# Kernel optimization log

Measured on AMD Instinct MI355X. Metric: run time of the kernel, lower is better.

## Reference

```python
import jax, jax.numpy as jnp
import numpy as np

B, P, G = 16, 16000, 256          # images, RPN proposals, gt boxes per image
S = 512                           # batch_size_per_image
POS_FRAC = 0.25
FG_T, BG_T = 0.5, 0.5             # fg/bg IoU thresholds
NUM_CLASSES = 91
BOX_W = jnp.array([10.0, 10.0, 5.0, 5.0], jnp.float32)  # box_coder weights
BETA = 1.0 / 9.0                  # smooth_l1 beta


def _make_boxes(k, n, img=800.0, maxwh=200.0):
    k1, k2 = jax.random.split(k)
    xy = jax.random.uniform(k1, (B, n, 2)) * img
    wh = jax.random.uniform(k2, (B, n, 2)) * maxwh + 1.0
    return jnp.concatenate([xy, xy + wh], -1)


def setup_inputs() -> dict:
    key = jax.random.key(0)
    ks = jax.random.split(key, 6)
    proposals = _make_boxes(ks[0], P)
    gt_boxes = _make_boxes(ks[1], G)
    gt_labels = jax.random.randint(ks[2], (B, G), 1, NUM_CLASSES)
    gt_thetas = jax.random.uniform(ks[3], (B, G)) * np.pi
    class_logits = jax.random.normal(ks[4], (B * S, NUM_CLASSES))
    box_regression = jax.random.normal(ks[5], (B * S, NUM_CLASSES * 5))
    return dict(class_logits=class_logits, box_regression=box_regression,
                proposals=proposals, gt_boxes=gt_boxes,
                gt_thetas=gt_thetas, gt_labels=gt_labels)


def _box_iou(a, b):
    # a: [G,4] gt, b: [M,4] proposals -> [G,M]
    area_a = (a[:, 2] - a[:, 0]) * (a[:, 3] - a[:, 1])
    area_b = (b[:, 2] - b[:, 0]) * (b[:, 3] - b[:, 1])
    lt = jnp.maximum(a[:, None, :2], b[None, :, :2])
    rb = jnp.minimum(a[:, None, 2:], b[None, :, 2:])
    wh = jnp.clip(rb - lt, 0.0)
    inter = wh[..., 0] * wh[..., 1]
    return inter / (area_a[:, None] + area_b[None, :] - inter)


def _encode(ref, prop):
    pw = prop[:, 2] - prop[:, 0]; ph = prop[:, 3] - prop[:, 1]
    px = prop[:, 0] + 0.5 * pw;   py = prop[:, 1] + 0.5 * ph
    gw = ref[:, 2] - ref[:, 0];   gh = ref[:, 3] - ref[:, 1]
    gx = ref[:, 0] + 0.5 * gw;    gy = ref[:, 1] + 0.5 * gh
    t = jnp.stack([(gx - px) / pw, (gy - py) / ph,
                   jnp.log(gw / pw), jnp.log(gh / ph)], 1)
    return t * BOX_W[None, :]


def _select_training_samples(props, gtb, gtl, gtt):
    # add_gt_proposals
    props_all = jnp.concatenate([props, gtb], 0)        # [P+G,4]
    # assign_targets_to_proposals (Matcher, allow_low_quality=False)
    iou = _box_iou(gtb, props_all)                      # [G,P+G]
    vals = iou.max(0)
    matches = iou.argmax(0)                             # clamped matched idxs
    below = vals < BG_T
    between = (vals >= BG_T) & (vals < FG_T)
    lbl = gtl[matches]
    lbl = jnp.where(below, 0, lbl)      # background
    lbl = jnp.where(between, -1, lbl)   # ignored
    # BalancedPositiveNegativeSampler (deterministic first-k variant)
    pos = lbl > 0
    neg = lbl == 0
    n_pos = jnp.minimum(pos.sum(), int(S * POS_FRAC))
    sel_pos = pos & (jnp.cumsum(pos) <= n_pos)
    sel_neg = neg & (jnp.cumsum(neg) <= (S - n_pos))
    mask = sel_pos | sel_neg
    sampled = jnp.argsort((~mask).astype(jnp.int32), stable=True)[:S]  # sorted selected idxs
    props_s = props_all[sampled]
    lbl_s = lbl[sampled]
    m = matches[sampled]
    reg = _encode(gtb[m], props_s)                       # [S,4]
    reg_t = jnp.concatenate([reg, gtt[m][:, None]], 1)   # append theta -> [S,5]
    return lbl_s, reg_t


def _fastrcnn_loss(class_logits, box_regression, labels, reg_targets):
    N = class_logits.shape[0]
    logp = jax.nn.log_softmax(class_logits, -1)
    cls_loss = -jnp.take_along_axis(logp, labels[:, None], 1).mean()
    br = box_regression.reshape(N, -1, 5)
    idx = jnp.broadcast_to(labels[:, None, None], (N, 1, 5))
    pred = jnp.take_along_axis(br, idx, axis=1)[:, 0, :]
    d = pred - reg_targets
    ad = jnp.abs(d)
    sl1 = jnp.where(ad < BETA, 0.5 * d * d / BETA, ad - 0.5 * BETA)
    pos = (labels > 0).astype(sl1.dtype)
    box_loss = jnp.sum(sl1 * pos[:, None]) / N
    return jnp.stack([cls_loss, box_loss])


def reference(class_logits, box_regression, proposals, gt_boxes, gt_thetas, gt_labels):
    labels, reg_t = jax.vmap(_select_training_samples)(proposals, gt_boxes, gt_labels, gt_thetas)
    labels = labels.reshape(-1)
    reg_t = reg_t.reshape(-1, 5)
    return _fastrcnn_loss(class_logits, box_regression, labels, reg_t)
```

## Files before the change

### kernel.cpp

```cpp
#include <hip/hip_runtime.h>

#define NB 16
#define NP 16000
#define NG 256
#define NM (NP + NG)
#define NSTRIP 254
#define NS 512
#define NCLS 91
#define SL1_BETA (1.0f/9.0f)
#define LOSS_BLOCKS 512

__global__ __launch_bounds__(256) void match_kernel(
    const float4* __restrict__ props4,
    const float4* __restrict__ gt4,
    const int*    __restrict__ gt_labels,
    unsigned int* __restrict__ posinfo)
{
    __shared__ float4   gbox[NG];
    __shared__ float    gar[NG];
    __shared__ int      glab[NG];
    __shared__ unsigned qst[256][5];

    const int b   = blockIdx.y;
    const int tid = threadIdx.x;

    {
        const float4 v = gt4[(size_t)b * NG + tid];
        gbox[tid] = v;
        gar[tid]  = (v.z - v.x) * (v.w - v.y);
        glab[tid] = gt_labels[b * NG + tid];
    }
    __syncthreads();

    const int h     = tid & 1;
    const int p     = tid >> 1;
    const int j     = blockIdx.x * 128 + p;
    const int gbase = h * 128;

    const float4 pb = (j < NP) ? props4[(size_t)b * NP + j]
                               : gt4[(size_t)b * NG + (j - NP)];
    const float ap = (pb.z - pb.x) * (pb.w - pb.y);

    int qcnt = 0, gf = -1;
    for (int w = 0; w < 4; ++w) {
        unsigned m = 0;
        #pragma unroll
        for (int t = 0; t < 32; ++t) {
            const int g = gbase + w * 32 + t;
            const float4 gb = gbox[g];
            const float  ga = gar[g];
            float lx = fmaxf(gb.x, pb.x), ly = fmaxf(gb.y, pb.y);
            float rx = fminf(gb.z, pb.z), ry = fminf(gb.w, pb.w);
            float ww = fmaxf(rx - lx, 0.0f), hh = fmaxf(ry - ly, 0.0f);
            float inter = ww * hh;
            float tt = ga + ap;
            if (fmaf(inter, 3.0f, -tt) >= 0.0f) m |= (1u << t);
        }
        qst[tid][w] = m;
        if (qcnt == 0 && m) gf = w * 32 + (__ffs(m) - 1);
        qcnt += __popc(m);
    }

    float ib = -1.0f, ub = 1.0f;
    int   gstar = -1;
    if (qcnt == 1) {
        const int g = gbase + gf;
        const float4 gb = gbox[g];
        float lx = fmaxf(gb.x, pb.x), ly = fmaxf(gb.y, pb.y);
        float rx = fminf(gb.z, pb.z), ry = fminf(gb.w, pb.w);
        float ww = fmaxf(rx - lx, 0.0f), hh = fmaxf(ry - ly, 0.0f);
        ib = ww * hh;
        ub = (gar[g] + ap) - ib;
        gstar = g;
    } else if (qcnt > 1) {
        for (int w = 0; w < 4; ++w) {
            unsigned m = qst[tid][w];
            while (m) {
                int t = __ffs(m) - 1; m &= m - 1;
                int g = gbase + w * 32 + t;
                const float4 gb = gbox[g];
                float lx = fmaxf(gb.x, pb.x), ly = fmaxf(gb.y, pb.y);
                float rx = fminf(gb.z, pb.z), ry = fminf(gb.w, pb.w);
                float ww = fmaxf(rx - lx, 0.0f), hh = fmaxf(ry - ly, 0.0f);
                float inter = ww * hh;
                float u = (gar[g] + ap) - inter;
                if (inter * ub > ib * u) { ib = inter; ub = u; gstar = g; }
            }
        }
    }

    const int   oq  = __shfl_xor(qcnt, 1, 64);
    const float oib = __shfl_xor(ib, 1, 64);
    const float oub = __shfl_xor(ub, 1, 64);
    const int   og  = __shfl_xor(gstar, 1, 64);
    const int qtot = qcnt + oq;
    int gm;
    if (qcnt > 0 && oq > 0) {
        bool otherWins;
        if (h == 0) otherWins = (oib * ub > ib * oub);
        else        otherWins = !(ib * oub > oib * ub);
        gm = otherWins ? og : gstar;
    } else {
        gm = (qcnt > 0) ? gstar : og;
    }

    if (h == 0) {
        unsigned info = 0;
        if (qtot > 0) info = ((unsigned)gm << 16) | (unsigned)glab[gm];
        posinfo[(size_t)b * NM + j] = info;
    }
}

__global__ __launch_bounds__(256) void sample_kernel(
    const float4* __restrict__ props4,
    const float4* __restrict__ gt4,
    const float*  __restrict__ gt_thetas,
    const unsigned int* __restrict__ posinfo,
    int*   __restrict__ labels_out,
    float* __restrict__ regt_out)
{
    __shared__ int sampled[NS];
    __shared__ int wsum[4];

    const int b    = blockIdx.x;
    const int tid  = threadIdx.x;
    const int lane = tid & 63;
    const int wid  = tid >> 6;
    const unsigned* P = posinfo + (size_t)b * NM;
    const int base = tid * 64;

    unsigned long long pm = 0ull;
    int cn = 0;
    if (tid < NSTRIP) {
        const uint4* Pv = reinterpret_cast<const uint4*>(P + base);
        #pragma unroll
        for (int q = 0; q < 16; ++q) {
            uint4 v = Pv[q];
            int e = q * 4;
            if (v.x) pm |= 1ull << (e + 0);
            if (v.y) pm |= 1ull << (e + 1);
            if (v.z) pm |= 1ull << (e + 2);
            if (v.w) pm |= 1ull << (e + 3);
        }
        cn = 64 - __popcll(pm);
    }
    int cp = (tid < NSTRIP) ? __popcll(pm) : 0;
    int val  = (cp << 16) | cn;
    int incl = val;
    #pragma unroll
    for (int off = 1; off < 64; off <<= 1) {
        int u = __shfl_up(incl, off, 64);
        if (lane >= off) incl += u;
    }
    if (lane == 63) wsum[wid] = incl;
    __syncthreads();
    int wbase = 0;
    #pragma unroll
    for (int w = 0; w < 4; ++w) if (w < wid) wbase += wsum[w];
    int tot  = wsum[0] + wsum[1] + wsum[2] + wsum[3];
    int excl = wbase + incl - val;
    int rp = excl >> 16, rn = excl & 0xffff;
    int posT = tot >> 16, negT = tot & 0xffff;
    int np = posT < 128 ? posT : 128;
    int nn = NS - np; if (nn > negT) nn = negT;

    if (tid < NSTRIP) {
        #pragma unroll 4
        for (int e = 0; e < 64; ++e) {
            int idx = base + e;
            if ((pm >> e) & 1ull) {
                if (rp < np) sampled[rp + (rn < nn ? rn : nn)] = idx;
                rp++;
            } else {
                if (rn < nn) sampled[rn + (rp < np ? rp : np)] = idx;
                rn++;
            }
        }
    }
    __syncthreads();
    if (tid == 0 && np + nn < NS) {
        int cpp = 0, cnn = 0, i = np + nn;
        for (int idx = 0; idx < NM && i < NS; ++idx) {
            bool p = P[idx] != 0;
            bool sel;
            if (p) { sel = cpp < np; cpp++; } else { sel = cnn < nn; cnn++; }
            if (!sel) sampled[i++] = idx;
        }
    }
    __syncthreads();

    for (int i = tid; i < NS; i += 256) {
        int idx = sampled[i];
        unsigned info = P[idx];
        int lbl = 0;
        if (info) {
            int m = info >> 16; lbl = info & 0xffff;
            float4 pv = (idx < NP) ? props4[(size_t)b * NP + idx]
                                   : gt4[(size_t)b * NG + (idx - NP)];
            float4 rv = gt4[(size_t)b * NG + m];
            float pw = pv.z - pv.x, ph = pv.w - pv.y;
            float px = pv.x + 0.5f * pw, py = pv.y + 0.5f * ph;
            float gw = rv.z - rv.x, gh = rv.w - rv.y;
            float gx = rv.x + 0.5f * gw, gy = rv.y + 0.5f * gh;
            float* o = regt_out + ((size_t)b * NS + i) * 5;
            o[0] = 10.0f * (gx - px) / pw;
            o[1] = 10.0f * (gy - py) / ph;
            o[2] = 5.0f * logf(gw / pw);
            o[3] = 5.0f * logf(gh / ph);
            o[4] = gt_thetas[b * NG + m];
        }
        labels_out[b * NS + i] = lbl;
    }
}

__global__ __launch_bounds__(256) void loss_kernel(
    const float* __restrict__ logits,
    const float* __restrict__ boxreg,
    const int*   __restrict__ labels,
    const float* __restrict__ regt,
    float2* __restrict__ partials)
{
    const int wave  = threadIdx.x >> 6;
    const int lane  = threadIdx.x & 63;
    const int gwave = blockIdx.x * 4 + wave;
    const int NWAVE = LOSS_BLOCKS * 4;
    const int N     = NB * NS;

    float cls_acc = 0.0f, box_acc = 0.0f;

    for (int r = gwave; r < N; r += NWAVE) {
        const float* row = logits + (size_t)r * NCLS;
        float a = (lane < NCLS)      ? row[lane]      : -3.0e38f;
        float c = (lane + 64 < NCLS) ? row[lane + 64] : -3.0e38f;
        float mx = fmaxf(a, c);
        #pragma unroll
        for (int o = 32; o; o >>= 1) mx = fmaxf(mx, __shfl_xor(mx, o, 64));
        float ssum = 0.0f;
        if (lane < NCLS)      ssum += expf(a - mx);
        if (lane + 64 < NCLS) ssum += expf(c - mx);
        #pragma unroll
        for (int o = 32; o; o >>= 1) ssum += __shfl_xor(ssum, o, 64);

        int lab = labels[r];
        float xl = (lab < 64) ? __shfl(a, lab, 64) : __shfl(c, lab - 64, 64);
        if (lane == 0) cls_acc += -(xl - mx - logf(ssum));

        if (lab > 0) {
            float d = 0.0f;
            if (lane < 5) {
                float pv = boxreg[(size_t)r * (NCLS * 5) + lab * 5 + lane];
                float tv = regt[(size_t)r * 5 + lane];
                d = pv - tv;
            }
            float ad = fabsf(d);
            float sl = (ad < SL1_BETA) ? 0.5f * d * d / SL1_BETA : ad - 0.5f * SL1_BETA;
            sl += __shfl_xor(sl, 4, 8);
            sl += __shfl_xor(sl, 2, 8);
            sl += __shfl_xor(sl, 1, 8);
            if (lane == 0) box_acc += sl;
        }
    }

    __shared__ float cpart[4], bpart[4];
    if (lane == 0) { cpart[wave] = cls_acc; bpart[wave] = box_acc; }
    __syncthreads();
    if (threadIdx.x == 0) {
        partials[blockIdx.x] = make_float2(cpart[0] + cpart[1] + cpart[2] + cpart[3],
                                           bpart[0] + bpart[1] + bpart[2] + bpart[3]);
    }
}

__global__ void final_kernel(const float2* __restrict__ partials,
                             float* __restrict__ out)
{
    const int tid  = threadIdx.x;
    const int lane = tid & 63;
    const int wid  = tid >> 6;
    float2 v0 = partials[tid];
    float2 v1 = partials[tid + 256];
    float c = v0.x + v1.x, bx = v0.y + v1.y;
    #pragma unroll
    for (int o = 32; o; o >>= 1) {
        c  += __shfl_xor(c, o, 64);
        bx += __shfl_xor(bx, o, 64);
    }
    __shared__ float cc[4], bb[4];
    if (lane == 0) { cc[wid] = c; bb[wid] = bx; }
    __syncthreads();
    if (tid == 0) {
        const float invN = 1.0f / (float)(NB * NS);
        out[0] = (cc[0] + cc[1] + cc[2] + cc[3]) * invN;
        out[1] = (bb[0] + bb[1] + bb[2] + bb[3]) * invN;
    }
}

extern "C" void kernel_launch(void* const* d_in, const int* in_sizes, int n_in,
                              void* d_out, int out_size, void* d_ws, size_t ws_size,
                              hipStream_t stream)
{
    const float* class_logits   = (const float*)d_in[0];
    const float* box_regression = (const float*)d_in[1];
    const float4* props4        = (const float4*)d_in[2];
    const float4* gt4           = (const float4*)d_in[3];
    const float* gt_thetas      = (const float*)d_in[4];
    const int*   gt_labels      = (const int*)d_in[5];
    float* out = (float*)d_out;

    char* ws = (char*)d_ws;
    unsigned int* posinfo = (unsigned int*)ws;
    float2* partials = (float2*)(ws + (((size_t)NB * NM * 4 + 255) & ~255ull));
    int* labs   = (int*)((char*)partials + ((LOSS_BLOCKS * sizeof(float2) + 255) & ~255ull));
    float* regt = (float*)(labs + (size_t)NB * NS);

    hipLaunchKernelGGL(match_kernel, dim3(127, NB), dim3(256), 0, stream,
                       props4, gt4, gt_labels, posinfo);
    hipLaunchKernelGGL(sample_kernel, dim3(NB), dim3(256), 0, stream,
                       props4, gt4, gt_thetas, posinfo, labs, regt);
    hipLaunchKernelGGL(loss_kernel, dim3(LOSS_BLOCKS), dim3(256), 0, stream,
                       class_logits, box_regression, labs, regt, partials);
    hipLaunchKernelGGL(final_kernel, dim3(1), dim3(256), 0, stream, partials, out);
}
```

Before: 54.69 us.

## Fuse match/sample via last-block atomics and overlap logsumexp with matching

Merges the match and sample kernels into one launch. The last block to finish each image, detected with an atomic counter, runs the sampling step. Extra blocks in the same grid compute the per-row logsumexp of the class logits alongside the IoU matching. The loss kernel becomes one thread per row using the precomputed stats, with a last-block final reduction replacing the separate final kernel. This cuts four launches to two plus a memset, at the cost of threadfence/atomic handshakes and serialized sampling work in the tail block per image.

```diff
diff --git a/kernel.cpp b/kernel.cpp
--- a/kernel.cpp
+++ b/kernel.cpp
@@ -8,37 +8,73 @@
 #define NS 512
 #define NCLS 91
 #define SL1_BETA (1.0f/9.0f)
-#define LOSS_BLOCKS 512
-
-__global__ __launch_bounds__(256) void match_kernel(
+#define MATCH_BLOCKS (127 * NB)
+#define STATS_BLOCKS 32
+#define K1_BLOCKS (MATCH_BLOCKS + STATS_BLOCKS)
+#define K2_BLOCKS 32
+
+__global__ __launch_bounds__(256) void k1_kernel(
     const float4* __restrict__ props4,
     const float4* __restrict__ gt4,
     const int*    __restrict__ gt_labels,
-    unsigned int* __restrict__ posinfo)
+    const float*  __restrict__ gt_thetas,
+    const float*  __restrict__ logits,
+    unsigned int* __restrict__ posinfo,
+    float*        __restrict__ stats,
+    unsigned int* __restrict__ imgcnt,
+    int*          __restrict__ labels_out,
+    float*        __restrict__ regt_out)
 {
+    const int bid = blockIdx.x;
+    const int tid = threadIdx.x;
+    const int lane = tid & 63;
+    const int wid  = tid >> 6;
+
+    if (bid >= MATCH_BLOCKS) {
+        const int gw = (bid - MATCH_BLOCKS) * 4 + wid;
+        for (int r = gw; r < NB * NS; r += STATS_BLOCKS * 4) {
+            const float* row = logits + (size_t)r * NCLS;
+            float a = (lane < NCLS)      ? row[lane]      : -3.0e38f;
+            float c = (lane + 64 < NCLS) ? row[lane + 64] : -3.0e38f;
+            float mx = fmaxf(a, c);
+            #pragma unroll
+            for (int o = 32; o; o >>= 1) mx = fmaxf(mx, __shfl_xor(mx, o, 64));
+            float ss = 0.0f;
+            if (lane < NCLS)      ss += expf(a - mx);
+            if (lane + 64 < NCLS) ss += expf(c - mx);
+            #pragma unroll
+            for (int o = 32; o; o >>= 1) ss += __shfl_xor(ss, o, 64);
+            if (lane == 0) stats[r] = mx + logf(ss);
+        }
+        return;
+    }
+
     __shared__ float4   gbox[NG];
     __shared__ float    gar[NG];
     __shared__ int      glab[NG];
     __shared__ unsigned qst[256][5];
-
-    const int b   = blockIdx.y;
-    const int tid = threadIdx.x;
+    __shared__ int      sampled[NS];
+    __shared__ int      wsum[4];
+    __shared__ int      amLast;
+
+    const int img = bid / 127;
+    const int s   = bid % 127;
 
     {
-        const float4 v = gt4[(size_t)b * NG + tid];
+        const float4 v = gt4[(size_t)img * NG + tid];
         gbox[tid] = v;
         gar[tid]  = (v.z - v.x) * (v.w - v.y);
-        glab[tid] = gt_labels[b * NG + tid];
+        glab[tid] = gt_labels[img * NG + tid];
     }
     __syncthreads();
 
     const int h     = tid & 1;
     const int p     = tid >> 1;
-    const int j     = blockIdx.x * 128 + p;
+    const int j     = s * 128 + p;
     const int gbase = h * 128;
 
-    const float4 pb = (j < NP) ? props4[(size_t)b * NP + j]
-                               : gt4[(size_t)b * NG + (j - NP)];
+    const float4 pb = (j < NP) ? props4[(size_t)img * NP + j]
+                               : gt4[(size_t)img * NG + (j - NP)];
     const float ap = (pb.z - pb.x) * (pb.w - pb.y);
 
     int qcnt = 0, gf = -1;
@@ -107,26 +143,20 @@
     if (h == 0) {
         unsigned info = 0;
         if (qtot > 0) info = ((unsigned)gm << 16) | (unsigned)glab[gm];
-        posinfo[(size_t)b * NM + j] = info;
-    }
-}
-
-__global__ __launch_bounds__(256) void sample_kernel(
-    const float4* __restrict__ props4,
-    const float4* __restrict__ gt4,
-    const float*  __restrict__ gt_thetas,
-    const unsigned int* __restrict__ posinfo,
-    int*   __restrict__ labels_out,
-    float* __restrict__ regt_out)
-{
-    __shared__ int sampled[NS];
-    __shared__ int wsum[4];
-
-    const int b    = blockIdx.x;
-    const int tid  = threadIdx.x;
-    const int lane = tid & 63;
-    const int wid  = tid >> 6;
-    const unsigned* P = posinfo + (size_t)b * NM;
+        posinfo[(size_t)img * NM + j] = info;
+    }
+
+    __syncthreads();
+    if (tid == 0) {
+        __threadfence();
+        unsigned old = atomicAdd(&imgcnt[img * 32], 1u);
+        amLast = (old == 126u);
+    }
+    __syncthreads();
+    if (!amLast) return;
+    __threadfence();
+
+    const unsigned* P = posinfo + (size_t)img * NM;
     const int base = tid * 64;
 
     unsigned long long pm = 0ull;
@@ -181,9 +211,9 @@
     if (tid == 0 && np + nn < NS) {
         int cpp = 0, cnn = 0, i = np + nn;
         for (int idx = 0; idx < NM && i < NS; ++idx) {
-            bool p = P[idx] != 0;
+            bool pp = P[idx] != 0;
             bool sel;
-            if (p) { sel = cpp < np; cpp++; } else { sel = cnn < nn; cnn++; }
+            if (pp) { sel = cpp < np; cpp++; } else { sel = cnn < nn; cnn++; }
             if (!sel) sampled[i++] = idx;
         }
     }
@@ -195,102 +225,83 @@
         int lbl = 0;
         if (info) {
             int m = info >> 16; lbl = info & 0xffff;
-            float4 pv = (idx < NP) ? props4[(size_t)b * NP + idx]
-                                   : gt4[(size_t)b * NG + (idx - NP)];
-            float4 rv = gt4[(size_t)b * NG + m];
+            float4 pv = (idx < NP) ? props4[(size_t)img * NP + idx]
+                                   : gt4[(size_t)img * NG + (idx - NP)];
+            float4 rv = gt4[(size_t)img * NG + m];
             float pw = pv.z - pv.x, ph = pv.w - pv.y;
             float px = pv.x + 0.5f * pw, py = pv.y + 0.5f * ph;
             float gw = rv.z - rv.x, gh = rv.w - rv.y;
             float gx = rv.x + 0.5f * gw, gy = rv.y + 0.5f * gh;
-            float* o = regt_out + ((size_t)b * NS + i) * 5;
+            float* o = regt_out + ((size_t)img * NS + i) * 5;
             o[0] = 10.0f * (gx - px) / pw;
             o[1] = 10.0f * (gy - py) / ph;
             o[2] = 5.0f * logf(gw / pw);
             o[3] = 5.0f * logf(gh / ph);
-            o[4] = gt_thetas[b * NG + m];
-        }
-        labels_out[b * NS + i] = lbl;
+            o[4] = gt_thetas[img * NG + m];
+        }
+        labels_out[img * NS + i] = lbl;
     }
 }
 
-__global__ __launch_bounds__(256) void loss_kernel(
+__global__ __launch_bounds__(256) void k2_kernel(
     const float* __restrict__ logits,
     const float* __restrict__ boxreg,
-    const int*   __restrict__ labels,
+    const int*   __restrict__ labs,
     const float* __restrict__ regt,
-    float2* __restrict__ partials)
-{
-    const int wave  = threadIdx.x >> 6;
-    const int lane  = threadIdx.x & 63;
-    const int gwave = blockIdx.x * 4 + wave;
-    const int NWAVE = LOSS_BLOCKS * 4;
-    const int N     = NB * NS;
-
-    float cls_acc = 0.0f, box_acc = 0.0f;
-
-    for (int r = gwave; r < N; r += NWAVE) {
-        const float* row = logits + (size_t)r * NCLS;
-        float a = (lane < NCLS)      ? row[lane]      : -3.0e38f;
-        float c = (lane + 64 < NCLS) ? row[lane + 64] : -3.0e38f;
-        float mx = fmaxf(a, c);
-        #pragma unroll
-        for (int o = 32; o; o >>= 1) mx = fmaxf(mx, __shfl_xor(mx, o, 64));
-        float ssum = 0.0f;
-        if (lane < NCLS)      ssum += expf(a - mx);
-        if (lane + 64 < NCLS) ssum += expf(c - mx);
-        #pragma unroll
-        for (int o = 32; o; o >>= 1) ssum += __shfl_xor(ssum, o, 64);
-
-        int lab = labels[r];
-        float xl = (lab < 64) ? __shfl(a, lab, 64) : __shfl(c, lab - 64, 64);
-        if (lane == 0) cls_acc += -(xl - mx - logf(ssum));
-
-        if (lab > 0) {
-            float d = 0.0f;
-            if (lane < 5) {
-                float pv = boxreg[(size_t)r * (NCLS * 5) + lab * 5 + lane];
-                float tv = regt[(size_t)r * 5 + lane];
-                d = pv - tv;
-            }
-            float ad = fabsf(d);
-            float sl = (ad < SL1_BETA) ? 0.5f * d * d / SL1_BETA : ad - 0.5f * SL1_BETA;
-            sl += __shfl_xor(sl, 4, 8);
-            sl += __shfl_xor(sl, 2, 8);
-            sl += __shfl_xor(sl, 1, 8);
-            if (lane == 0) box_acc += sl;
-        }
-    }
-
-    __shared__ float cpart[4], bpart[4];
-    if (lane == 0) { cpart[wave] = cls_acc; bpart[wave] = box_acc; }
-    __syncthreads();
-    if (threadIdx.x == 0) {
-        partials[blockIdx.x] = make_float2(cpart[0] + cpart[1] + cpart[2] + cpart[3],
-                                           bpart[0] + bpart[1] + bpart[2] + bpart[3]);
-    }
-}
-
-__global__ void final_kernel(const float2* __restrict__ partials,
-                             float* __restrict__ out)
+    const float* __restrict__ stats,
+    float2* __restrict__ partials,
+    unsigned int* __restrict__ cnt2,
+    float* __restrict__ out)
 {
     const int tid  = threadIdx.x;
     const int lane = tid & 63;
     const int wid  = tid >> 6;
-    float2 v0 = partials[tid];
-    float2 v1 = partials[tid + 256];
-    float c = v0.x + v1.x, bx = v0.y + v1.y;
+    const int r    = blockIdx.x * 256 + tid;
+
+    const int lab = labs[r];
+    float cls = stats[r] - logits[(size_t)r * NCLS + lab];
+    float box = 0.0f;
+    if (lab > 0) {
+        const float* pr = boxreg + (size_t)r * (NCLS * 5) + lab * 5;
+        const float* tg = regt + (size_t)r * 5;
+        #pragma unroll
+        for (int k = 0; k < 5; ++k) {
+            float d  = pr[k] - tg[k];
+            float ad = fabsf(d);
+            box += (ad < SL1_BETA) ? 0.5f * d * d / SL1_BETA : ad - 0.5f * SL1_BETA;
+        }
+    }
     #pragma unroll
     for (int o = 32; o; o >>= 1) {
-        c  += __shfl_xor(c, o, 64);
-        bx += __shfl_xor(bx, o, 64);
+        cls += __shfl_xor(cls, o, 64);
+        box += __shfl_xor(box, o, 64);
     }
     __shared__ float cc[4], bb[4];
-    if (lane == 0) { cc[wid] = c; bb[wid] = bx; }
+    __shared__ int last;
+    if (lane == 0) { cc[wid] = cls; bb[wid] = box; }
     __syncthreads();
     if (tid == 0) {
-        const float invN = 1.0f / (float)(NB * NS);
-        out[0] = (cc[0] + cc[1] + cc[2] + cc[3]) * invN;
-        out[1] = (bb[0] + bb[1] + bb[2] + bb[3]) * invN;
+        partials[blockIdx.x] = make_float2(cc[0] + cc[1] + cc[2] + cc[3],
+                                           bb[0] + bb[1] + bb[2] + bb[3]);
+        __threadfence();
+        last = (atomicAdd(cnt2, 1u) == K2_BLOCKS - 1);
+    }
+    __syncthreads();
+    if (!last) return;
+    __threadfence();
+    if (tid < 64) {
+        float2 v = (tid < K2_BLOCKS) ? partials[tid] : make_float2(0.f, 0.f);
+        float c = v.x, bx = v.y;
+        #pragma unroll
+        for (int o = 32; o; o >>= 1) {
+            c  += __shfl_xor(c, o, 64);
+            bx += __shfl_xor(bx, o, 64);
+        }
+        if (tid == 0) {
+            const float invN = 1.0f / (float)(NB * NS);
+            out[0] = c * invN;
+            out[1] = bx * invN;
+        }
     }
 }
 
@@ -307,16 +318,20 @@
     float* out = (float*)d_out;
 
     char* ws = (char*)d_ws;
-    unsigned int* posinfo = (unsigned int*)ws;
-    float2* partials = (float2*)(ws + (((size_t)NB * NM * 4 + 255) & ~255ull));
-    int* labs   = (int*)((char*)partials + ((LOSS_BLOCKS * sizeof(float2) + 255) & ~255ull));
-    float* regt = (float*)(labs + (size_t)NB * NS);
-
-    hipLaunchKernelGGL(match_kernel, dim3(127, NB), dim3(256), 0, stream,
-                       props4, gt4, gt_labels, posinfo);
-    hipLaunchKernelGGL(sample_kernel, dim3(NB), dim3(256), 0, stream,
-                       props4, gt4, gt_thetas, posinfo, labs, regt);
-    hipLaunchKernelGGL(loss_kernel, dim3(LOSS_BLOCKS), dim3(256), 0, stream,
-                       class_logits, box_regression, labs, regt, partials);
-    hipLaunchKernelGGL(final_kernel, dim3(1), dim3(256), 0, stream, partials, out);
+    unsigned int* imgcnt = (unsigned int*)ws;
+    unsigned int* cnt2   = (unsigned int*)(ws + 2048);
+    unsigned int* posinfo = (unsigned int*)(ws + 4096);
+    char* pend = ws + 4096 + (((size_t)NB * NM * 4 + 255) & ~255ull);
+    float* stats = (float*)pend;
+    int*   labs  = (int*)(pend + ((size_t)NB * NS * 4 + 256 & ~255ull));
+    float* regt  = (float*)((char*)labs + ((size_t)NB * NS * 4 + 256 & ~255ull));
+    float2* partials = (float2*)((char*)regt + ((size_t)NB * NS * 5 * 4 + 256 & ~255ull));
+
+    hipMemsetAsync(ws, 0, 4096, stream);
+    hipLaunchKernelGGL(k1_kernel, dim3(K1_BLOCKS), dim3(256), 0, stream,
+                       props4, gt4, gt_labels, gt_thetas, class_logits,
+                       posinfo, stats, imgcnt, labs, regt);
+    hipLaunchKernelGGL(k2_kernel, dim3(K2_BLOCKS), dim3(256), 0, stream,
+                       class_logits, box_regression, labs, regt, stats,
+                       partials, cnt2, out);
 }
```

New measurement: 107.6 us. 96.7% more time.

## Rewrite matching with register-broadcast GT boxes and fuse final reduction

Applied to the files above, without the earlier changes.

The match kernel no longer stages GT boxes in shared memory with a two-pass bitmask scheme. Each thread now handles two proposals and computes a full argmax over all 256 GT boxes, broadcasting GT coordinates through readlane from registers. The final-reduction kernel is removed: the loss kernel uses an atomic counter so the last block sums the partials, and the loss block count drops to 128. This trades shared-memory traffic, the second pass and one launch for more IoU compares and divergent argmax updates per thread. Running 32x16 match blocks may also underfill the GPU.

```diff
diff --git a/kernel.cpp b/kernel.cpp
--- a/kernel.cpp
+++ b/kernel.cpp
@@ -8,106 +8,92 @@
 #define NS 512
 #define NCLS 91
 #define SL1_BETA (1.0f/9.0f)
-#define LOSS_BLOCKS 512
+#define LOSS_BLOCKS 128
+
+__device__ __forceinline__ float rlf(float v, int l) {
+    return __int_as_float(__builtin_amdgcn_readlane(__float_as_int(v), l));
+}
 
 __global__ __launch_bounds__(256) void match_kernel(
     const float4* __restrict__ props4,
     const float4* __restrict__ gt4,
     const int*    __restrict__ gt_labels,
-    unsigned int* __restrict__ posinfo)
+    unsigned int* __restrict__ posinfo,
+    unsigned int* __restrict__ cnt2)
 {
-    __shared__ float4   gbox[NG];
-    __shared__ float    gar[NG];
-    __shared__ int      glab[NG];
-    __shared__ unsigned qst[256][5];
-
-    const int b   = blockIdx.y;
-    const int tid = threadIdx.x;
+    const int b    = blockIdx.y;
+    const int tid  = threadIdx.x;
+    const int lane = tid & 63;
+    if (blockIdx.x == 0 && b == 0 && tid == 0) *cnt2 = 0;
+
+    const float4 g0 = gt4[(size_t)b * NG + lane];
+    const float4 g1 = gt4[(size_t)b * NG + 64 + lane];
+    const float4 g2 = gt4[(size_t)b * NG + 128 + lane];
+    const float4 g3 = gt4[(size_t)b * NG + 192 + lane];
+    const float  a0 = (g0.z - g0.x) * (g0.w - g0.y);
+    const float  a1 = (g1.z - g1.x) * (g1.w - g1.y);
+    const float  a2 = (g2.z - g2.x) * (g2.w - g2.y);
+    const float  a3 = (g3.z - g3.x) * (g3.w - g3.y);
+
+    const int jA = blockIdx.x * 512 + tid;
+    const int jB = jA + 256;
+    const bool vB = (jB < NM);
+
+    const float4 pA = (jA < NP) ? props4[(size_t)b * NP + jA]
+                                : gt4[(size_t)b * NG + (jA - NP)];
+    float4 pB = make_float4(0.f, 0.f, 0.f, 0.f);
+    if (vB) pB = (jB < NP) ? props4[(size_t)b * NP + jB]
+                           : gt4[(size_t)b * NG + (jB - NP)];
+    const float apA = (pA.z - pA.x) * (pA.w - pA.y);
+    const float apB = (pB.z - pB.x) * (pB.w - pB.y);
+
+    float ibA = -1.f, ubA = 1.f, tA = 0.f;  int gA = 0;
+    float ibB = -1.f, ubB = 1.f, tB = 0.f;  int gB = 0;
+
+#define GT_GROUP(GV, AV, KBASE)                                              \
+    for (int l = 0; l < 64; ++l) {                                           \
+        const float gx0 = rlf(GV.x, l), gy0 = rlf(GV.y, l);                  \
+        const float gx1 = rlf(GV.z, l), gy1 = rlf(GV.w, l);                  \
+        const float ga  = rlf(AV, l);                                        \
+        {                                                    \
+            float lx = fmaxf(gx0, pA.x), ly = fmaxf(gy0, pA.y);              \
+            float rx = fminf(gx1, pA.z), ry = fminf(gy1, pA.w);              \
+            float w  = fmaxf(rx - lx, 0.f), h = fmaxf(ry - ly, 0.f);         \
+            float inter = w * h;                                             \
+            float t = ga + apA;                                              \
+            float u = t - inter;                                             \
+            if (inter * ubA > ibA * u) {                                     \
+                ibA = inter; ubA = u; tA = t; gA = (KBASE) + l; }            \
+        }                                                                    \
+        {                                                    \
+            float lx = fmaxf(gx0, pB.x), ly = fmaxf(gy0, pB.y);              \
+            float rx = fminf(gx1, pB.z), ry = fminf(gy1, pB.w);              \
+            float w  = fmaxf(rx - lx, 0.f), h = fmaxf(ry - ly, 0.f);         \
+            float inter = w * h;                                             \
+            float t = ga + apB;                                              \
+            float u = t - inter;                                             \
+            if (inter * ubB > ibB * u) {                                     \
+                ibB = inter; ubB = u; tB = t; gB = (KBASE) + l; }            \
+        }                                                                    \
+    }
+
+    GT_GROUP(g0, a0, 0)
+    GT_GROUP(g1, a1, 64)
+    GT_GROUP(g2, a2, 128)
+    GT_GROUP(g3, a3, 192)
+#undef GT_GROUP
 
     {
-        const float4 v = gt4[(size_t)b * NG + tid];
-        gbox[tid] = v;
-        gar[tid]  = (v.z - v.x) * (v.w - v.y);
-        glab[tid] = gt_labels[b * NG + tid];
-    }
-    __syncthreads();
-
-    const int h     = tid & 1;
-    const int p     = tid >> 1;
-    const int j     = blockIdx.x * 128 + p;
-    const int gbase = h * 128;
-
-    const float4 pb = (j < NP) ? props4[(size_t)b * NP + j]
-                               : gt4[(size_t)b * NG + (j - NP)];
-    const float ap = (pb.z - pb.x) * (pb.w - pb.y);
-
-    int qcnt = 0, gf = -1;
-    for (int w = 0; w < 4; ++w) {
-        unsigned m = 0;
-        #pragma unroll
-        for (int t = 0; t < 32; ++t) {
-            const int g = gbase + w * 32 + t;
-            const float4 gb = gbox[g];
-            const float  ga = gar[g];
-            float lx = fmaxf(gb.x, pb.x), ly = fmaxf(gb.y, pb.y);
-            float rx = fminf(gb.z, pb.z), ry = fminf(gb.w, pb.w);
-            float ww = fmaxf(rx - lx, 0.0f), hh = fmaxf(ry - ly, 0.0f);
-            float inter = ww * hh;
-            float tt = ga + ap;
-            if (fmaf(inter, 3.0f, -tt) >= 0.0f) m |= (1u << t);
-        }
-        qst[tid][w] = m;
-        if (qcnt == 0 && m) gf = w * 32 + (__ffs(m) - 1);
-        qcnt += __popc(m);
-    }
-
-    float ib = -1.0f, ub = 1.0f;
-    int   gstar = -1;
-    if (qcnt == 1) {
-        const int g = gbase + gf;
-        const float4 gb = gbox[g];
-        float lx = fmaxf(gb.x, pb.x), ly = fmaxf(gb.y, pb.y);
-        float rx = fminf(gb.z, pb.z), ry = fminf(gb.w, pb.w);
-        float ww = fmaxf(rx - lx, 0.0f), hh = fmaxf(ry - ly, 0.0f);
-        ib = ww * hh;
-        ub = (gar[g] + ap) - ib;
-        gstar = g;
-    } else if (qcnt > 1) {
-        for (int w = 0; w < 4; ++w) {
-            unsigned m = qst[tid][w];
-            while (m) {
-                int t = __ffs(m) - 1; m &= m - 1;
-                int g = gbase + w * 32 + t;
-                const float4 gb = gbox[g];
-                float lx = fmaxf(gb.x, pb.x), ly = fmaxf(gb.y, pb.y);
-                float rx = fminf(gb.z, pb.z), ry = fminf(gb.w, pb.w);
-                float ww = fmaxf(rx - lx, 0.0f), hh = fmaxf(ry - ly, 0.0f);
-                float inter = ww * hh;
-                float u = (gar[g] + ap) - inter;
-                if (inter * ub > ib * u) { ib = inter; ub = u; gstar = g; }
-            }
-        }
-    }
-
-    const int   oq  = __shfl_xor(qcnt, 1, 64);
-    const float oib = __shfl_xor(ib, 1, 64);
-    const float oub = __shfl_xor(ub, 1, 64);
-    const int   og  = __shfl_xor(gstar, 1, 64);
-    const int qtot = qcnt + oq;
-    int gm;
-    if (qcnt > 0 && oq > 0) {
-        bool otherWins;
-        if (h == 0) otherWins = (oib * ub > ib * oub);
-        else        otherWins = !(ib * oub > oib * ub);
-        gm = otherWins ? og : gstar;
-    } else {
-        gm = (qcnt > 0) ? gstar : og;
-    }
-
-    if (h == 0) {
         unsigned info = 0;
-        if (qtot > 0) info = ((unsigned)gm << 16) | (unsigned)glab[gm];
-        posinfo[(size_t)b * NM + j] = info;
+        if (fmaf(ibA, 3.0f, -tA) >= 0.0f)
+            info = ((unsigned)gA << 16) | (unsigned)gt_labels[b * NG + gA];
+        posinfo[(size_t)b * NM + jA] = info;
+    }
+    if (vB) {
+        unsigned info = 0;
+        if (fmaf(ibB, 3.0f, -tB) >= 0.0f)
+            info = ((unsigned)gB << 16) | (unsigned)gt_labels[b * NG + gB];
+        posinfo[(size_t)b * NM + jB] = info;
     }
 }
 
@@ -218,7 +204,9 @@
     const float* __restrict__ boxreg,
     const int*   __restrict__ labels,
     const float* __restrict__ regt,
-    float2* __restrict__ partials)
+    float2* __restrict__ partials,
+    unsigned int* __restrict__ cnt2,
+    float* __restrict__ out)
 {
     const int wave  = threadIdx.x >> 6;
     const int lane  = threadIdx.x & 63;
@@ -262,35 +250,33 @@
     }
 
     __shared__ float cpart[4], bpart[4];
+    __shared__ int amLast;
     if (lane == 0) { cpart[wave] = cls_acc; bpart[wave] = box_acc; }
     __syncthreads();
     if (threadIdx.x == 0) {
         partials[blockIdx.x] = make_float2(cpart[0] + cpart[1] + cpart[2] + cpart[3],
                                            bpart[0] + bpart[1] + bpart[2] + bpart[3]);
-    }
-}
-
-__global__ void final_kernel(const float2* __restrict__ partials,
-                             float* __restrict__ out)
-{
-    const int tid  = threadIdx.x;
-    const int lane = tid & 63;
-    const int wid  = tid >> 6;
-    float2 v0 = partials[tid];
-    float2 v1 = partials[tid + 256];
-    float c = v0.x + v1.x, bx = v0.y + v1.y;
-    #pragma unroll
-    for (int o = 32; o; o >>= 1) {
-        c  += __shfl_xor(c, o, 64);
-        bx += __shfl_xor(bx, o, 64);
-    }
-    __shared__ float cc[4], bb[4];
-    if (lane == 0) { cc[wid] = c; bb[wid] = bx; }
-    __syncthreads();
-    if (tid == 0) {
-        const float invN = 1.0f / (float)(NB * NS);
-        out[0] = (cc[0] + cc[1] + cc[2] + cc[3]) * invN;
-        out[1] = (bb[0] + bb[1] + bb[2] + bb[3]) * invN;
+        __threadfence();
+        amLast = (atomicAdd(cnt2, 1u) == LOSS_BLOCKS - 1);
+    }
+    __syncthreads();
+    if (!amLast) return;
+    __threadfence();
+    if (threadIdx.x < 64) {
+        const int tid = threadIdx.x;
+        float2 v0 = partials[tid];
+        float2 v1 = partials[tid + 64];
+        float c = v0.x + v1.x, bx = v0.y + v1.y;
+        #pragma unroll
+        for (int o = 32; o; o >>= 1) {
+            c  += __shfl_xor(c, o, 64);
+            bx += __shfl_xor(bx, o, 64);
+        }
+        if (tid == 0) {
+            const float invN = 1.0f / (float)(NB * NS);
+            out[0] = c * invN;
+            out[1] = bx * invN;
+        }
     }
 }
 
@@ -307,16 +293,17 @@
     float* out = (float*)d_out;
 
     char* ws = (char*)d_ws;
-    unsigned int* posinfo = (unsigned int*)ws;
-    float2* partials = (float2*)(ws + (((size_t)NB * NM * 4 + 255) & ~255ull));
-    int* labs   = (int*)((char*)partials + ((LOSS_BLOCKS * sizeof(float2) + 255) & ~255ull));
-    float* regt = (float*)(labs + (size_t)NB * NS);
-
-    hipLaunchKernelGGL(match_kernel, dim3(127, NB), dim3(256), 0, stream,
-                       props4, gt4, gt_labels, posinfo);
+    unsigned int* cnt2 = (unsigned int*)ws;
+    unsigned int* posinfo = (unsigned int*)(ws + 256);
+    char* pend = ws + 256 + (((size_t)NB * NM * 4 + 255) & ~255ull);
+    int*   labs  = (int*)pend;
+    float* regt  = (float*)(pend + (((size_t)NB * NS * 4 + 255) & ~255ull));
+    float2* partials = (float2*)((char*)regt + (((size_t)NB * NS * 5 * 4 + 255) & ~255ull));
+
+    hipLaunchKernelGGL(match_kernel, dim3(32, NB), dim3(256), 0, stream,
+                       props4, gt4, gt_labels, posinfo, cnt2);
     hipLaunchKernelGGL(sample_kernel, dim3(NB), dim3(256), 0, stream,
                        props4, gt4, gt_thetas, posinfo, labs, regt);
     hipLaunchKernelGGL(loss_kernel, dim3(LOSS_BLOCKS), dim3(256), 0, stream,
-                       class_logits, box_regression, labs, regt, partials);
-    hipLaunchKernelGGL(final_kernel, dim3(1), dim3(256), 0, stream, partials, out);
-}
+                       class_logits, box_regression, labs, regt, partials, cnt2, out);
+}
```

Result: slower. 84.37 us (+54.3%).

## Precompute logsumexp in match kernel, simplify IoU argmax, thin loss kernel

Applied to the files above, without the earlier changes.

Extra blocks in the match kernel now compute per-row logsumexp of the class logits, which removes that work from the dependent loss kernel. The loss kernel becomes one thread per row reading the precomputed stat, and the final reduction shrinks to 32 partials. The match loop is replaced with a single-pass argmax over all GT boxes, applying the threshold test only to the winner, and the bitmask/second-pass logic is dropped. The risk is that the full-argmax loop does division-free comparisons for every GT and may cost more ALU than the sparse two-pass scheme did.

```diff
diff --git a/kernel.cpp b/kernel.cpp
--- a/kernel.cpp
+++ b/kernel.cpp
@@ -8,105 +8,92 @@
 #define NS 512
 #define NCLS 91
 #define SL1_BETA (1.0f/9.0f)
-#define LOSS_BLOCKS 512
-
-__global__ __launch_bounds__(256) void match_kernel(
+#define MATCHX 127
+#define STATSX 4
+
+__global__ __launch_bounds__(256) void k1_kernel(
     const float4* __restrict__ props4,
     const float4* __restrict__ gt4,
     const int*    __restrict__ gt_labels,
-    unsigned int* __restrict__ posinfo)
-{
-    __shared__ float4   gbox[NG];
-    __shared__ float    gar[NG];
-    __shared__ int      glab[NG];
-    __shared__ unsigned qst[256][5];
-
-    const int b   = blockIdx.y;
-    const int tid = threadIdx.x;
+    const float*  __restrict__ logits,
+    unsigned int* __restrict__ posinfo,
+    float*        __restrict__ stats)
+{
+    const int b    = blockIdx.y;
+    const int bx   = blockIdx.x;
+    const int tid  = threadIdx.x;
+    const int lane = tid & 63;
+    const int wid  = tid >> 6;
+
+    if (bx >= MATCHX) {
+        const int sid = (bx - MATCHX) * NB + b;
+        for (int rr = 0; rr < 32; ++rr) {
+            const int r = sid * 128 + wid * 32 + rr;
+            const float* row = logits + (size_t)r * NCLS;
+            float a = (lane < NCLS)      ? row[lane]      : -3.0e38f;
+            float c = (lane + 64 < NCLS) ? row[lane + 64] : -3.0e38f;
+            float mx = fmaxf(a, c);
+            #pragma unroll
+            for (int o = 32; o; o >>= 1) mx = fmaxf(mx, __shfl_xor(mx, o, 64));
+            float ss = 0.0f;
+            if (lane < NCLS)      ss += expf(a - mx);
+            if (lane + 64 < NCLS) ss += expf(c - mx);
+            #pragma unroll
+            for (int o = 32; o; o >>= 1) ss += __shfl_xor(ss, o, 64);
+            if (lane == 0) stats[r] = mx + logf(ss);
+        }
+        return;
+    }
+
+    __shared__ float4 gbox[NG];
+    __shared__ float  gar[NG];
 
     {
         const float4 v = gt4[(size_t)b * NG + tid];
         gbox[tid] = v;
         gar[tid]  = (v.z - v.x) * (v.w - v.y);
-        glab[tid] = gt_labels[b * NG + tid];
     }
     __syncthreads();
 
     const int h     = tid & 1;
-    const int p     = tid >> 1;
-    const int j     = blockIdx.x * 128 + p;
+    const int j     = bx * 128 + (tid >> 1);
     const int gbase = h * 128;
 
     const float4 pb = (j < NP) ? props4[(size_t)b * NP + j]
                                : gt4[(size_t)b * NG + (j - NP)];
     const float ap = (pb.z - pb.x) * (pb.w - pb.y);
 
-    int qcnt = 0, gf = -1;
-    for (int w = 0; w < 4; ++w) {
-        unsigned m = 0;
-        #pragma unroll
-        for (int t = 0; t < 32; ++t) {
-            const int g = gbase + w * 32 + t;
-            const float4 gb = gbox[g];
-            const float  ga = gar[g];
-            float lx = fmaxf(gb.x, pb.x), ly = fmaxf(gb.y, pb.y);
-            float rx = fminf(gb.z, pb.z), ry = fminf(gb.w, pb.w);
-            float ww = fmaxf(rx - lx, 0.0f), hh = fmaxf(ry - ly, 0.0f);
-            float inter = ww * hh;
-            float tt = ga + ap;
-            if (fmaf(inter, 3.0f, -tt) >= 0.0f) m |= (1u << t);
-        }
-        qst[tid][w] = m;
-        if (qcnt == 0 && m) gf = w * 32 + (__ffs(m) - 1);
-        qcnt += __popc(m);
-    }
-
-    float ib = -1.0f, ub = 1.0f;
-    int   gstar = -1;
-    if (qcnt == 1) {
-        const int g = gbase + gf;
+    float ib = -1.0f, ub = 1.0f, tt = 0.0f;
+    int   gs = 0;
+    #pragma unroll 4
+    for (int k = 0; k < 128; ++k) {
+        const int g = gbase + k;
         const float4 gb = gbox[g];
+        const float  ga = gar[g];
         float lx = fmaxf(gb.x, pb.x), ly = fmaxf(gb.y, pb.y);
         float rx = fminf(gb.z, pb.z), ry = fminf(gb.w, pb.w);
-        float ww = fmaxf(rx - lx, 0.0f), hh = fmaxf(ry - ly, 0.0f);
-        ib = ww * hh;
-        ub = (gar[g] + ap) - ib;
-        gstar = g;
-    } else if (qcnt > 1) {
-        for (int w = 0; w < 4; ++w) {
-            unsigned m = qst[tid][w];
-            while (m) {
-                int t = __ffs(m) - 1; m &= m - 1;
-                int g = gbase + w * 32 + t;
-                const float4 gb = gbox[g];
-                float lx = fmaxf(gb.x, pb.x), ly = fmaxf(gb.y, pb.y);
-                float rx = fminf(gb.z, pb.z), ry = fminf(gb.w, pb.w);
-                float ww = fmaxf(rx - lx, 0.0f), hh = fmaxf(ry - ly, 0.0f);
-                float inter = ww * hh;
-                float u = (gar[g] + ap) - inter;
-                if (inter * ub > ib * u) { ib = inter; ub = u; gstar = g; }
-            }
-        }
-    }
-
-    const int   oq  = __shfl_xor(qcnt, 1, 64);
+        float w  = fmaxf(rx - lx, 0.0f), hh = fmaxf(ry - ly, 0.0f);
+        float inter = w * hh;
+        float t = ga + ap;
+        float u = t - inter;
+        if (inter * ub > ib * u) { ib = inter; ub = u; tt = t; gs = g; }
+    }
+
     const float oib = __shfl_xor(ib, 1, 64);
     const float oub = __shfl_xor(ub, 1, 64);
-    const int   og  = __shfl_xor(gstar, 1, 64);
-    const int qtot = qcnt + oq;
-    int gm;
-    if (qcnt > 0 && oq > 0) {
-        bool otherWins;
-        if (h == 0) otherWins = (oib * ub > ib * oub);
-        else        otherWins = !(ib * oub > oib * ub);
-        gm = otherWins ? og : gstar;
-    } else {
-        gm = (qcnt > 0) ? gstar : og;
-    }
+    const float ott = __shfl_xor(tt, 1, 64);
+    const int   og  = __shfl_xor(gs, 1, 64);
+    bool otherWins;
+    if (h == 0) otherWins = (oib * ub > ib * oub);
+    else        otherWins = !(ib * oub > oib * ub);
+    const float fib = otherWins ? oib : ib;
+    const float ftt = otherWins ? ott : tt;
+    const int   fgm = otherWins ? og  : gs;
 
     if (h == 0) {
         unsigned info = 0;
-        if (qtot > 0) info = ((unsigned)gm << 16) | (unsigned)glab[gm];
+        if (fmaf(fib, 3.0f, -ftt) >= 0.0f)
+            info = ((unsigned)fgm << 16) | (unsigned)gt_labels[b * NG + fgm];
         posinfo[(size_t)b * NM + j] = info;
     }
 }
@@ -216,81 +203,57 @@
 __global__ __launch_bounds__(256) void loss_kernel(
     const float* __restrict__ logits,
     const float* __restrict__ boxreg,
-    const int*   __restrict__ labels,
+    const int*   __restrict__ labs,
     const float* __restrict__ regt,
+    const float* __restrict__ stats,
     float2* __restrict__ partials)
-{
-    const int wave  = threadIdx.x >> 6;
-    const int lane  = threadIdx.x & 63;
-    const int gwave = blockIdx.x * 4 + wave;
-    const int NWAVE = LOSS_BLOCKS * 4;
-    const int N     = NB * NS;
-
-    float cls_acc = 0.0f, box_acc = 0.0f;
-
-    for (int r = gwave; r < N; r += NWAVE) {
-        const float* row = logits + (size_t)r * NCLS;
-        float a = (lane < NCLS)      ? row[lane]      : -3.0e38f;
-        float c = (lane + 64 < NCLS) ? row[lane + 64] : -3.0e38f;
-        float mx = fmaxf(a, c);
-        #pragma unroll
-        for (int o = 32; o; o >>= 1) mx = fmaxf(mx, __shfl_xor(mx, o, 64));
-        float ssum = 0.0f;
-        if (lane < NCLS)      ssum += expf(a - mx);
-        if (lane + 64 < NCLS) ssum += expf(c - mx);
-        #pragma unroll
-        for (int o = 32; o; o >>= 1) ssum += __shfl_xor(ssum, o, 64);
-
-        int lab = labels[r];
-        float xl = (lab < 64) ? __shfl(a, lab, 64) : __shfl(c, lab - 64, 64);
-        if (lane == 0) cls_acc += -(xl - mx - logf(ssum));
-
-        if (lab > 0) {
-            float d = 0.0f;
-            if (lane < 5) {
-                float pv = boxreg[(size_t)r * (NCLS * 5) + lab * 5 + lane];
-                float tv = regt[(size_t)r * 5 + lane];
-                d = pv - tv;
-            }
-            float ad = fabsf(d);
-            float sl = (ad < SL1_BETA) ? 0.5f * d * d / SL1_BETA : ad - 0.5f * SL1_BETA;
-            sl += __shfl_xor(sl, 4, 8);
-            sl += __shfl_xor(sl, 2, 8);
-            sl += __shfl_xor(sl, 1, 8);
-            if (lane == 0) box_acc += sl;
-        }
-    }
-
-    __shared__ float cpart[4], bpart[4];
-    if (lane == 0) { cpart[wave] = cls_acc; bpart[wave] = box_acc; }
-    __syncthreads();
-    if (threadIdx.x == 0) {
-        partials[blockIdx.x] = make_float2(cpart[0] + cpart[1] + cpart[2] + cpart[3],
-                                           bpart[0] + bpart[1] + bpart[2] + bpart[3]);
-    }
-}
-
-__global__ void final_kernel(const float2* __restrict__ partials,
-                             float* __restrict__ out)
 {
     const int tid  = threadIdx.x;
     const int lane = tid & 63;
     const int wid  = tid >> 6;
-    float2 v0 = partials[tid];
-    float2 v1 = partials[tid + 256];
-    float c = v0.x + v1.x, bx = v0.y + v1.y;
+    const int r    = blockIdx.x * 256 + tid;
+
+    const int lab = labs[r];
+    float cls = stats[r] - logits[(size_t)r * NCLS + lab];
+    float box = 0.0f;
+    if (lab > 0) {
+        const float* pr = boxreg + (size_t)r * (NCLS * 5) + lab * 5;
+        const float* tg = regt + (size_t)r * 5;
+        #pragma unroll
+        for (int k = 0; k < 5; ++k) {
+            float d  = pr[k] - tg[k];
+            float ad = fabsf(d);
+            box += (ad < SL1_BETA) ? 0.5f * d * d / SL1_BETA : ad - 0.5f * SL1_BETA;
+        }
+    }
+    #pragma unroll
+    for (int o = 32; o; o >>= 1) {
+        cls += __shfl_xor(cls, o, 64);
+        box += __shfl_xor(box, o, 64);
+    }
+    __shared__ float cc[4], bb[4];
+    if (lane == 0) { cc[wid] = cls; bb[wid] = box; }
+    __syncthreads();
+    if (tid == 0)
+        partials[blockIdx.x] = make_float2(cc[0] + cc[1] + cc[2] + cc[3],
+                                           bb[0] + bb[1] + bb[2] + bb[3]);
+}
+
+__global__ void final_kernel(const float2* __restrict__ partials,
+                             float* __restrict__ out)
+{
+    const int tid = threadIdx.x;
+    float2 v = (tid < 32) ? partials[tid] : make_float2(0.f, 0.f);
+    float c = v.x, bx = v.y;
     #pragma unroll
     for (int o = 32; o; o >>= 1) {
         c  += __shfl_xor(c, o, 64);
         bx += __shfl_xor(bx, o, 64);
     }
-    __shared__ float cc[4], bb[4];
-    if (lane == 0) { cc[wid] = c; bb[wid] = bx; }
-    __syncthreads();
     if (tid == 0) {
         const float invN = 1.0f / (float)(NB * NS);
-        out[0] = (cc[0] + cc[1] + cc[2] + cc[3]) * invN;
-        out[1] = (bb[0] + bb[1] + bb[2] + bb[3]) * invN;
+        out[0] = c * invN;
+        out[1] = bx * invN;
     }
 }
 
@@ -308,15 +271,17 @@
 
     char* ws = (char*)d_ws;
     unsigned int* posinfo = (unsigned int*)ws;
-    float2* partials = (float2*)(ws + (((size_t)NB * NM * 4 + 255) & ~255ull));
-    int* labs   = (int*)((char*)partials + ((LOSS_BLOCKS * sizeof(float2) + 255) & ~255ull));
-    float* regt = (float*)(labs + (size_t)NB * NS);
-
-    hipLaunchKernelGGL(match_kernel, dim3(127, NB), dim3(256), 0, stream,
-                       props4, gt4, gt_labels, posinfo);
+    char* pend = ws + (((size_t)NB * NM * 4 + 255) & ~255ull);
+    float* stats = (float*)pend;
+    int*   labs  = (int*)(pend + (((size_t)NB * NS * 4 + 255) & ~255ull));
+    float* regt  = (float*)((char*)labs + (((size_t)NB * NS * 4 + 255) & ~255ull));
+    float2* partials = (float2*)((char*)regt + (((size_t)NB * NS * 5 * 4 + 255) & ~255ull));
+
+    hipLaunchKernelGGL(k1_kernel, dim3(MATCHX + STATSX, NB), dim3(256), 0, stream,
+                       props4, gt4, gt_labels, class_logits, posinfo, stats);
     hipLaunchKernelGGL(sample_kernel, dim3(NB), dim3(256), 0, stream,
                        props4, gt4, gt_thetas, posinfo, labs, regt);
-    hipLaunchKernelGGL(loss_kernel, dim3(LOSS_BLOCKS), dim3(256), 0, stream,
-                       class_logits, box_regression, labs, regt, partials);
-    hipLaunchKernelGGL(final_kernel, dim3(1), dim3(256), 0, stream, partials, out);
-}
+    hipLaunchKernelGGL(loss_kernel, dim3(32), dim3(256), 0, stream,
+                       class_logits, box_regression, labs, regt, stats, partials);
+    hipLaunchKernelGGL(final_kernel, dim3(1), dim3(64), 0, stream, partials, out);
+}
```

After: 71.63 us. 1.31x slower.
